# Kernel tuning notes

Measured on AMD Instinct MI355X. Metric: run time of the kernel, lower is better.

The kernel has to match this reference:

```python
import jax, jax.numpy as jnp
import numpy as np

CONF_THRES = 0.2   # from __init__ default
IOU_THRES = 0.6    # from __init__ default
MAX_WH = 4096.0    # class-offset for multi-class NMS (yolov7 convention)
TOPK = 2048        # pre-NMS candidates per image
MAX_DET = 300      # max detections per image (yolov7 default)
B, N, NC = 8, 25200, 80


def setup_inputs() -> dict:
    key = jax.random.key(0)
    k1, k2, k3 = jax.random.split(key, 3)
    # decoded predictions: [cx, cy, w, h, obj, cls_0..cls_79]
    xywh = jax.random.uniform(k1, (B, N, 4)) * jnp.array([640.0, 640.0, 120.0, 120.0])
    obj = jax.random.uniform(k2, (B, N, 1))
    cls = jax.random.uniform(k3, (B, N, NC))
    preds = jnp.concatenate([xywh, obj, cls], axis=-1)  # [B, N, 85]
    return {"preds": preds}


def _xywh2xyxy(xywh):
    cx, cy, w, h = xywh[..., 0], xywh[..., 1], xywh[..., 2], xywh[..., 3]
    return jnp.stack([cx - w * 0.5, cy - h * 0.5, cx + w * 0.5, cy + h * 0.5], axis=-1)


def _box_iou(a, b):
    # a: [K,4], b: [K,4] -> [K,K] pairwise IoU
    area_a = (a[:, 2] - a[:, 0]) * (a[:, 3] - a[:, 1])
    area_b = (b[:, 2] - b[:, 0]) * (b[:, 3] - b[:, 1])
    lt = jnp.maximum(a[:, None, :2], b[None, :, :2])  # [K,K,2]
    rb = jnp.minimum(a[:, None, 2:], b[None, :, 2:])
    wh = jnp.clip(rb - lt, 0.0)
    inter = wh[..., 0] * wh[..., 1]
    return inter / (area_a[:, None] + area_b[None, :] - inter + 1e-9)


def _nms_single(pred):
    # pred: [N, 5+NC]
    boxes = _xywh2xyxy(pred[:, :4])                 # [N,4]
    scores_all = pred[:, 5:] * pred[:, 4:5]         # obj * cls  [N,NC]
    conf = jnp.max(scores_all, axis=-1)             # best-class conf
    cls_id = jnp.argmax(scores_all, axis=-1)
    scores = jnp.where(conf > CONF_THRES, conf, 0.0)

    # pre-NMS top-k candidates (sorted descending)
    top_scores, idx = jax.lax.top_k(scores, TOPK)
    top_boxes = boxes[idx]                          # [K,4]
    top_cls = cls_id[idx]                           # [K]
    top_valid = top_scores > CONF_THRES

    # per-class NMS via class offset so cross-class boxes never overlap
    offset_boxes = top_boxes + (top_cls.astype(top_boxes.dtype) * MAX_WH)[:, None]
    iou = _box_iou(offset_boxes, offset_boxes)      # [K,K]

    # greedy NMS over score-sorted candidates
    def body(i, state):
        keep, suppressed = state
        k_i = top_valid[i] & jnp.logical_not(suppressed[i])
        keep = keep.at[i].set(k_i)
        sup_new = suppressed | (k_i & (iou[i] > IOU_THRES))
        sup_new = sup_new.at[i].set(suppressed[i])  # never self-suppress
        return keep, sup_new

    keep, _ = jax.lax.fori_loop(
        0, TOPK, body,
        (jnp.zeros(TOPK, dtype=bool), jnp.zeros(TOPK, dtype=bool)))

    # take top MAX_DET kept detections
    keep_scores = jnp.where(keep, top_scores, -1.0)
    det_scores, det_idx = jax.lax.top_k(keep_scores, MAX_DET)
    det = jnp.concatenate(
        [top_boxes[det_idx],
         det_scores[:, None],
         top_cls[det_idx].astype(pred.dtype)[:, None]], axis=-1)  # [MAX_DET,6]
    det = jnp.where((det_scores > 0.0)[:, None], det, 0.0)
    return det


def reference(preds):
    # preds: [B, N, 5+NC] -> [B, MAX_DET, 6] (x1,y1,x2,y2,conf,cls), zero-padded
    return jax.vmap(_nms_single)(preds)
```

## Files before the change

kernel.cpp:

```cpp
#include <hip/hip_runtime.h>

#define BATCH 8
#define NPRED 25200
#define NCLS 80
#define ROWW 85
#define TOPKK 2048
#define MAXDET 300
#define CANDMAX 4096
#define NBUCKET 4096
#define CONF_T 0.2f
#define IOU_T 0.6f
#define CLS_OFF 4096.0f

#define MASKN 384
#define MCH (MASKN / 64)
#define MW 13

typedef unsigned long long u64;
typedef unsigned int u32;

__device__ __forceinline__ int bucket_of_key(u64 k) {
    float sc = __uint_as_float((u32)(k >> 32));
    int bkt = (int)(sc * (float)NBUCKET);
    return (bkt > NBUCKET - 1) ? (NBUCKET - 1) : bkt;
}

__global__ __launch_bounds__(256) void k_score(
    const float* __restrict__ preds,
    u64* __restrict__ keys,
    unsigned char* __restrict__ cls8,
    u32* __restrict__ hist_g)
{
    __shared__ float4 rows4[64 * ROWW / 4 + 4];
    const int t = threadIdx.x;
    const int lane = t & 63;
    const int wave = t >> 6;
    const size_t rowbase = (size_t)blockIdx.x * 64;
    const float4* src = reinterpret_cast<const float4*>(preds + rowbase * ROWW);

    for (int q = wave; q < 21; q += 4) {
        __builtin_amdgcn_global_load_lds(
            (const __attribute__((address_space(1))) void*)(src + q * 64 + lane),
            (__attribute__((address_space(3))) void*)(rows4 + q * 64),
            16, 0, 0);
    }
    if (t < 16) rows4[1344 + t] = src[1344 + t];
    __syncthreads();

    const float* rows = reinterpret_cast<const float*>(rows4);
    const int r = t >> 2;
    const int j = t & 3;
    const float* p = rows + r * ROWW;
    const float obj = p[4];

    float best = -1.0f;
    int bi = 0;
    #pragma unroll
    for (int tt = 0; tt < 20; ++tt) {
        int c = j + 4 * tt;
        float s = __fmul_rn(obj, p[5 + c]);
        if (s > best) { best = s; bi = c; }
    }
    #pragma unroll
    for (int d = 1; d <= 2; d <<= 1) {
        float os = __shfl_xor(best, d);
        int oi = __shfl_xor(bi, d);
        if (os > best || (os == best && oi < bi)) { best = os; bi = oi; }
    }

    if (j == 0) {
        unsigned gid = (unsigned)rowbase + r;
        u64 key = 0ull;
        if (best > CONF_T) {
            key = ((u64)__float_as_uint(best) << 32) | (0xFFFFFFFFu - (gid % NPRED));
        }
        keys[gid] = key;
        cls8[gid] = (unsigned char)bi;
        if (key) {
            atomicAdd(&hist_g[(gid / NPRED) * NBUCKET + bucket_of_key(key)], 1u);
        }
    }
}

__global__ __launch_bounds__(1024) void k_scan(
    const u32* __restrict__ hist_g,
    u32* __restrict__ bstart_g,
    u32* __restrict__ balloc_g,
    int* __restrict__ tb_g,
    u32* __restrict__ stored_g)
{
    __shared__ u32 wtot[16];
    __shared__ u32 wsuf[16];
    __shared__ int s_tb;
    __shared__ u32 s_stored;

    const int b = blockIdx.x;
    const int t = threadIdx.x;
    const int lane = t & 63;
    const int wave = t >> 6;
    const u32* H = hist_g + (size_t)b * NBUCKET;

    u32 h0 = H[4 * t], h1 = H[4 * t + 1], h2 = H[4 * t + 2], h3 = H[4 * t + 3];
    u32 ps = h0 + h1 + h2 + h3;

    u32 v = ps;
    #pragma unroll
    for (int off = 1; off < 64; off <<= 1) {
        u32 u2 = __shfl_down(v, off);
        if (lane + off < 64) v += u2;
    }
    if (lane == 0) wtot[wave] = v;
    __syncthreads();
    if (t < 16) {
        u32 w = wtot[t];
        u32 s = w;
        #pragma unroll
        for (int off = 1; off < 16; off <<= 1) {
            u32 u2 = __shfl_down(s, off);
            if (t + off < 16) s += u2;
        }
        wsuf[t] = s - w;
    }
    if (t == 0) s_tb = 0;
    __syncthreads();
    u32 suffix_t = v + wsuf[wave];
    u32 snext = suffix_t - ps;

    u32 b3 = snext;
    u32 b2 = b3 + h3;
    u32 b1 = b2 + h2;
    u32 b0 = b1 + h1;
    const size_t B0 = (size_t)b * NBUCKET;
    bstart_g[B0 + 4 * t + 0] = b0;
    bstart_g[B0 + 4 * t + 1] = b1;
    bstart_g[B0 + 4 * t + 2] = b2;
    bstart_g[B0 + 4 * t + 3] = b3;
    balloc_g[B0 + 4 * t + 0] = b0;
    balloc_g[B0 + 4 * t + 1] = b1;
    balloc_g[B0 + 4 * t + 2] = b2;
    balloc_g[B0 + 4 * t + 3] = b3;

    if (t == 0) s_stored = (suffix_t < (u32)CANDMAX) ? suffix_t : (u32)CANDMAX;
    __syncthreads();
    {
        u32 c3 = b3 + h3, c2 = b2 + h2, c1 = b1 + h1, c0 = b0 + h0;
        if (c3 >= TOPKK && b3 < TOPKK) { s_tb = 4 * t + 3; s_stored = (c3 < (u32)CANDMAX) ? c3 : (u32)CANDMAX; }
        if (c2 >= TOPKK && b2 < TOPKK) { s_tb = 4 * t + 2; s_stored = (c2 < (u32)CANDMAX) ? c2 : (u32)CANDMAX; }
        if (c1 >= TOPKK && b1 < TOPKK) { s_tb = 4 * t + 1; s_stored = (c1 < (u32)CANDMAX) ? c1 : (u32)CANDMAX; }
        if (c0 >= TOPKK && b0 < TOPKK) { s_tb = 4 * t + 0; s_stored = (c0 < (u32)CANDMAX) ? c0 : (u32)CANDMAX; }
    }
    __syncthreads();
    if (t == 0) { tb_g[b] = s_tb; stored_g[b] = s_stored; }
}

__global__ __launch_bounds__(256) void k_compact(
    const u64* __restrict__ keys,
    u32* __restrict__ balloc_g,
    const int* __restrict__ tb_g,
    u64* __restrict__ cand_g)
{
    unsigned gid = blockIdx.x * 256 + threadIdx.x;
    if (gid >= BATCH * NPRED) return;
    u64 k = keys[gid];
    if (!k) return;
    int b = gid / NPRED;
    int bkt = bucket_of_key(k);
    if (bkt < tb_g[b]) return;
    u32 slot = atomicAdd(&balloc_g[(size_t)b * NBUCKET + bkt], 1u);
    if (slot < CANDMAX) cand_g[(size_t)b * CANDMAX + slot] = k;
}

struct RankPhase {
    u32 histL[NBUCKET];
    u32 bstartL[NBUCKET];
};
struct NmsPhase {
    u32 masks32[MASKN * MW];
    float4 cbx[MASKN];
    float carea[MASKN];
    float4 kb[MAXDET];
};

__global__ __launch_bounds__(1024) void k_finish(
    const float* __restrict__ preds,
    const unsigned char* __restrict__ cls8,
    const u32* __restrict__ hist_g,
    const u32* __restrict__ bstart_g,
    const int* __restrict__ tb_g,
    const u32* __restrict__ stored_g,
    const u64* __restrict__ cand_g,
    float* __restrict__ out)
{
    __shared__ union { RankPhase rk; NmsPhase nms; } u;
    __shared__ u64 candL[CANDMAX];
    __shared__ unsigned short rank2cand[TOPKK];
    __shared__ float4 sbox[MASKN];
    __shared__ float sscore[MASKN];
    __shared__ float scls[MASKN];
    __shared__ u64 validw[MCH];

    const int b = blockIdx.x;
    const int t = threadIdx.x;
    const int lane = t & 63;
    const int wave = t >> 6;
    float* ob = out + (size_t)b * MAXDET * 6;
    const u32 stored = stored_g[b];
    const int tb = tb_g[b];

    for (int i = tb + t; i < NBUCKET; i += 1024) {
        u.rk.histL[i] = hist_g[(size_t)b * NBUCKET + i];
        u.rk.bstartL[i] = bstart_g[(size_t)b * NBUCKET + i];
    }
    for (int i = t; i < TOPKK; i += 1024) rank2cand[i] = 0xFFFFu;
    for (int i = t; i < CANDMAX; i += 1024)
        if ((u32)i < stored) candL[i] = cand_g[(size_t)b * CANDMAX + i];
    if (t < MASKN) {
        sbox[t] = make_float4(0.f, 0.f, 0.f, 0.f);
        sscore[t] = 0.f;
        scls[t] = 0.f;
    }
    __syncthreads();

    for (u32 i = t; i < stored; i += 1024) {
        u64 k = candL[i];
        int bkt = bucket_of_key(k);
        u32 base = u.rk.bstartL[bkt];
        u32 end = base + u.rk.histL[bkt];
        if (end > stored) end = stored;
        u32 r = base;
        for (u32 jx = base; jx < end; ++jx) r += (candL[jx] > k) ? 1u : 0u;
        if (r < TOPKK) rank2cand[r] = (unsigned short)i;
        if (r < MASKN) {
            float sc = __uint_as_float((u32)(k >> 32));
            unsigned idx = 0xFFFFFFFFu - (u32)(k & 0xFFFFFFFFu);
            const float* p = preds + ((size_t)b * NPRED + idx) * ROWW;
            float cx = p[0], cy = p[1], w = p[2], h = p[3];
            float hw = __fmul_rn(w, 0.5f);
            float hh = __fmul_rn(h, 0.5f);
            sbox[r] = make_float4(__fsub_rn(cx, hw), __fsub_rn(cy, hh),
                                  __fadd_rn(cx, hw), __fadd_rn(cy, hh));
            sscore[r] = sc;
            scls[r] = (float)cls8[(size_t)b * NPRED + idx];
        }
    }
    __syncthreads();

    if (t < MASKN) {
        float sc = sscore[t];
        float cl = scls[t];
        float4 bb = sbox[t];
        float off = __fmul_rn(cl, CLS_OFF);
        float4 obx = make_float4(__fadd_rn(bb.x, off), __fadd_rn(bb.y, off),
                                 __fadd_rn(bb.z, off), __fadd_rn(bb.w, off));
        u.nms.cbx[t] = obx;
        u.nms.carea[t] = __fmul_rn(__fsub_rn(obx.z, obx.x), __fsub_rn(obx.w, obx.y));
        u64 vb = __ballot(sc > CONF_T);
        if (lane == 0) validw[wave] = vb;
    }
    __syncthreads();

    for (int tu = 0; tu < 3; ++tu) {
        int uidx = wave + 16 * tu;
        if (uidx >= 42) break;
        int q, s;
        if (uidx < 12)      { q = 0; s = uidx; }
        else if (uidx < 22) { q = 1; s = uidx - 12 + 2; }
        else if (uidx < 30) { q = 2; s = uidx - 22 + 4; }
        else if (uidx < 36) { q = 3; s = uidx - 30 + 6; }
        else if (uidx < 40) { q = 4; s = uidx - 36 + 8; }
        else                { q = 5; s = uidx - 40 + 10; }

        const int r = q * 64 + lane;
        const float4 me = u.nms.cbx[r];
        const float aA = u.nms.carea[r];
        const int j0 = s * 32;
        u32 acc = 0u;
        #pragma unroll 8
        for (int jj = 0; jj < 32; ++jj) {
            const int jx = j0 + jj;
            float4 cb = u.nms.cbx[jx];
            float lx = fmaxf(me.x, cb.x), ly = fmaxf(me.y, cb.y);
            float rx = fminf(me.z, cb.z), ry = fminf(me.w, cb.w);
            float iw = fmaxf(__fsub_rn(rx, lx), 0.0f);
            float ih = fmaxf(__fsub_rn(ry, ly), 0.0f);
            float inter = __fmul_rn(iw, ih);
            float denom = __fadd_rn(__fsub_rn(__fadd_rn(aA, u.nms.carea[jx]), inter), 1e-9f);
            bool sv = inter > __fmul_rn(IOU_T, denom);
            acc |= ((u32)sv) << jj;
        }
        if (s == 2 * q || s == 2 * q + 1) {
            int shift = r - j0;
            u32 dm = (shift < 0) ? ~0u : ((shift >= 31) ? 0u : (~0u << (shift + 1)));
            acc &= dm;
        }
        u.nms.masks32[r * MW + s] = acc;
    }
    __syncthreads();
    if (wave != 0) return;

    const u64 below = (lane == 0) ? 0ull : (~0ull >> (64 - lane));
    u64 S[MCH];
    #pragma unroll
    for (int w = 0; w < MCH; ++w) S[w] = 0ull;
    int nk = 0;
    bool done = false, allfull = true;

    #pragma unroll
    for (int c = 0; c < MCH; ++c) {
        if (done) break;
        u64 vw = validw[c];
        u64 eligible = vw & ~S[c];
        const int rbase = (c * 64 + lane) * MW;
        u64 Mu = ((u64)u.nms.masks32[rbase + 2 * c + 1] << 32) |
                 (u64)u.nms.masks32[rbase + 2 * c];
        bool elig = (eligible >> lane) & 1ull;
        if (eligible) {
            int cap = MAXDET - nk;
            u64 edge = __ballot(elig && ((Mu & eligible) != 0ull));
            u64 keptm;
            if (edge == 0ull) {
                int rank = __popcll(eligible & below);
                keptm = __ballot(elig && (rank < cap));
            } else {
                u64 km = 0ull, supm = 0ull;
                int cnt = 0;
                for (int m = 0; m < 64 && cnt < cap; ++m) {
                    if (!((eligible >> m) & 1ull)) continue;
                    if ((supm >> m) & 1ull) continue;
                    km |= 1ull << m;
                    ++cnt;
                    supm |= __shfl(Mu, m);
                }
                keptm = km;
            }
            if ((keptm >> lane) & 1ull) {
                int pos = nk + __popcll(keptm & below);
                int i = c * 64 + lane;
                float4 bb = sbox[i];
                u.nms.kb[pos] = u.nms.cbx[i];
                float* row = ob + pos * 6;
                row[0] = bb.x; row[1] = bb.y; row[2] = bb.z; row[3] = bb.w;
                row[4] = sscore[i]; row[5] = scls[i];
            }
            nk += __popcll(keptm);
            if (nk >= MAXDET) {
                done = true;
            } else if (keptm) {
                for (int w = c + 1; w < MCH; ++w) {
                    u64 v2 = ((keptm >> lane) & 1ull)
                        ? (((u64)u.nms.masks32[rbase + 2 * w + 1] << 32) |
                           (u64)u.nms.masks32[rbase + 2 * w])
                        : 0ull;
                    v2 |= __shfl_xor(v2, 1);  v2 |= __shfl_xor(v2, 2);
                    v2 |= __shfl_xor(v2, 4);  v2 |= __shfl_xor(v2, 8);
                    v2 |= __shfl_xor(v2, 16); v2 |= __shfl_xor(v2, 32);
                    S[w] |= v2;
                }
            }
        }
        if (vw != ~0ull) { allfull = false; break; }
    }

    if (!done && allfull && nk < MAXDET) {
        __threadfence_block();
        for (int c = MCH; c < TOPKK / 64; ++c) {
            int r = c * 64 + lane;
            unsigned short ci = rank2cand[r];
            bool valid = (ci != 0xFFFFu);
            u64 validmask = __ballot(valid);
            if (validmask == 0ull) break;

            float sc = 0.f, cl = 0.f;
            float bx1 = 0.f, by1 = 0.f, bx2 = 0.f, by2 = 0.f;
            if (valid) {
                u64 k = candL[ci];
                sc = __uint_as_float((u32)(k >> 32));
                unsigned idx = 0xFFFFFFFFu - (u32)(k & 0xFFFFFFFFu);
                const float* p = preds + ((size_t)b * NPRED + idx) * ROWW;
                float cx = p[0], cy = p[1], w = p[2], h = p[3];
                float hw = __fmul_rn(w, 0.5f);
                float hh = __fmul_rn(h, 0.5f);
                bx1 = __fsub_rn(cx, hw); by1 = __fsub_rn(cy, hh);
                bx2 = __fadd_rn(cx, hw); by2 = __fadd_rn(cy, hh);
                cl = (float)cls8[(size_t)b * NPRED + idx];
            }
            float off = __fmul_rn(cl, CLS_OFF);
            float x1 = __fadd_rn(bx1, off), y1 = __fadd_rn(by1, off);
            float x2 = __fadd_rn(bx2, off), y2 = __fadd_rn(by2, off);
            float areaA = __fmul_rn(__fsub_rn(x2, x1), __fsub_rn(y2, y1));

            bool sup = false;
            for (int jx = 0; jx < nk; ++jx) {
                float4 k4 = u.nms.kb[jx];
                float lx = fmaxf(x1, k4.x), ly = fmaxf(y1, k4.y);
                float rx = fminf(x2, k4.z), ry = fminf(y2, k4.w);
                float iw = fmaxf(__fsub_rn(rx, lx), 0.0f);
                float ih = fmaxf(__fsub_rn(ry, ly), 0.0f);
                float inter = __fmul_rn(iw, ih);
                float areaB = __fmul_rn(__fsub_rn(k4.z, k4.x), __fsub_rn(k4.w, k4.y));
                float denom = __fadd_rn(__fsub_rn(__fadd_rn(areaA, areaB), inter), 1e-9f);
                if (inter > __fmul_rn(IOU_T, denom)) sup = true;
            }
            u64 supprev = __ballot(sup);

            u32 sb_lo = 0u, sb_hi = 0u;
            for (int m = 0; m < 64; ++m) {
                float mx1 = __shfl(x1, m), my1 = __shfl(y1, m);
                float mx2 = __shfl(x2, m), my2 = __shfl(y2, m);
                float lx = fmaxf(x1, mx1), ly = fmaxf(y1, my1);
                float rx = fminf(x2, mx2), ry = fminf(y2, my2);
                float iw = fmaxf(__fsub_rn(rx, lx), 0.0f);
                float ih = fmaxf(__fsub_rn(ry, ly), 0.0f);
                float inter = __fmul_rn(iw, ih);
                float areaB = __fmul_rn(__fsub_rn(mx2, mx1), __fsub_rn(my2, my1));
                float denom = __fadd_rn(__fsub_rn(__fadd_rn(areaA, areaB), inter), 1e-9f);
                bool s = (m != lane) && (inter > __fmul_rn(IOU_T, denom));
                if (m < 32) sb_lo |= ((u32)s) << m;
                else        sb_hi |= ((u32)s) << (m - 32);
            }

            u64 eligible = validmask & ~supprev;
            u64 mysb = (((u64)sb_hi << 32) | (u64)sb_lo);
            bool iselig = (eligible >> lane) & 1ull;
            u64 edgeball = __ballot(iselig && ((mysb & eligible & below) != 0ull));

            u64 keptm;
            int cap = MAXDET - nk;
            if (edgeball == 0ull) {
                int rank = __popcll(eligible & below);
                keptm = __ballot(iselig && (rank < cap));
            } else {
                u64 km = 0ull;
                int cnt = 0;
                for (int m = 0; m < 64 && cnt < cap; ++m) {
                    if (!((validmask >> m) & 1ull)) break;
                    if ((supprev >> m) & 1ull) continue;
                    u32 mlo = (u32)__shfl((int)sb_lo, m);
                    u32 mhi = (u32)__shfl((int)sb_hi, m);
                    u64 supby = (((u64)mhi << 32) | (u64)mlo);
                    if (supby & km) continue;
                    km |= 1ull << m;
                    ++cnt;
                }
                keptm = km;
            }

            if ((keptm >> lane) & 1ull) {
                int pos = nk + __popcll(keptm & below);
                u.nms.kb[pos] = make_float4(x1, y1, x2, y2);
                float* row = ob + pos * 6;
                row[0] = bx1; row[1] = by1; row[2] = bx2; row[3] = by2;
                row[4] = sc;  row[5] = cl;
            }
            __threadfence_block();
            nk += __popcll(keptm);
            if (nk >= MAXDET) break;
            if (validmask != ~0ull) break;
        }
    }

    for (int x = nk * 6 + lane; x < MAXDET * 6; x += 64) ob[x] = 0.0f;
}

extern "C" void kernel_launch(void* const* d_in, const int* in_sizes, int n_in,
                              void* d_out, int out_size, void* d_ws, size_t ws_size,
                              hipStream_t stream) {
    const float* preds = (const float*)d_in[0];
    float* out = (float*)d_out;

    u32* hist_g   = (u32*)d_ws;
    u32* bstart_g = hist_g + BATCH * NBUCKET;
    u32* balloc_g = bstart_g + BATCH * NBUCKET;
    int* tb_g     = (int*)(balloc_g + BATCH * NBUCKET);
    u32* stored_g = (u32*)(tb_g + 8);
    u64* keys     = (u64*)(stored_g + 8);
    unsigned char* cls8 = (unsigned char*)(keys + BATCH * NPRED);
    u64* cand_g   = (u64*)(cls8 + BATCH * NPRED);

    hipMemsetAsync(hist_g, 0, (size_t)BATCH * NBUCKET * sizeof(u32), stream);

    hipLaunchKernelGGL(k_score, dim3(BATCH * NPRED / 64), dim3(256), 0, stream,
                       preds, keys, cls8, hist_g);
    hipLaunchKernelGGL(k_scan, dim3(BATCH), dim3(1024), 0, stream,
                       hist_g, bstart_g, balloc_g, tb_g, stored_g);
    hipLaunchKernelGGL(k_compact, dim3((BATCH * NPRED + 255) / 256), dim3(256), 0, stream,
                       keys, balloc_g, tb_g, cand_g);
    hipLaunchKernelGGL(k_finish, dim3(BATCH), dim3(1024), 0, stream,
                       preds, cls8, hist_g, bstart_g, tb_g, stored_g, cand_g, out);
}
```

Measured before the change: 64.87 us.

## Build per-image score histogram in LDS inside scan kernel, drop global atomics and memset

Moves the bucket histogram from global atomics in k_score into shared-memory atomics inside k_scan, which rereads the keys per image. This removes the hipMemsetAsync launch and the global atomic traffic. k_compact now handles two keys per thread with 16-byte loads. k_finish derives bucket end positions from neighbouring bstart entries instead of loading the histogram. The trade-off is that k_scan runs on only 8 blocks and must stream about 200 KB of keys each, which may serialize work that was previously spread across the whole grid.

```diff
diff --git a/kernel.cpp b/kernel.cpp
--- a/kernel.cpp
+++ b/kernel.cpp
@@ -28,8 +28,7 @@
 __global__ __launch_bounds__(256) void k_score(
     const float* __restrict__ preds,
     u64* __restrict__ keys,
-    unsigned char* __restrict__ cls8,
-    u32* __restrict__ hist_g)
+    unsigned char* __restrict__ cls8)
 {
     __shared__ float4 rows4[64 * ROWW / 4 + 4];
     const int t = threadIdx.x;
@@ -76,19 +75,17 @@
         }
         keys[gid] = key;
         cls8[gid] = (unsigned char)bi;
-        if (key) {
-            atomicAdd(&hist_g[(gid / NPRED) * NBUCKET + bucket_of_key(key)], 1u);
-        }
     }
 }
 
 __global__ __launch_bounds__(1024) void k_scan(
-    const u32* __restrict__ hist_g,
+    const u64* __restrict__ keys,
     u32* __restrict__ bstart_g,
     u32* __restrict__ balloc_g,
     int* __restrict__ tb_g,
     u32* __restrict__ stored_g)
 {
+    __shared__ u32 histL[NBUCKET];
     __shared__ u32 wtot[16];
     __shared__ u32 wsuf[16];
     __shared__ int s_tb;
@@ -98,9 +95,21 @@
     const int t = threadIdx.x;
     const int lane = t & 63;
     const int wave = t >> 6;
-    const u32* H = hist_g + (size_t)b * NBUCKET;
-
-    u32 h0 = H[4 * t], h1 = H[4 * t + 1], h2 = H[4 * t + 2], h3 = H[4 * t + 3];
+
+    for (int i = t; i < NBUCKET; i += 1024) histL[i] = 0u;
+    __syncthreads();
+
+    const uint4* k4 = reinterpret_cast<const uint4*>(keys + (size_t)b * NPRED);
+    for (int i = t; i < NPRED / 2; i += 1024) {
+        uint4 v = k4[i];
+        u64 ka = ((u64)v.y << 32) | v.x;
+        u64 kb = ((u64)v.w << 32) | v.z;
+        if (ka) atomicAdd(&histL[bucket_of_key(ka)], 1u);
+        if (kb) atomicAdd(&histL[bucket_of_key(kb)], 1u);
+    }
+    __syncthreads();
+
+    u32 h0 = histL[4 * t], h1 = histL[4 * t + 1], h2 = histL[4 * t + 2], h3 = histL[4 * t + 3];
     u32 ps = h0 + h1 + h2 + h3;
 
     u32 v = ps;
@@ -159,19 +168,30 @@
     const int* __restrict__ tb_g,
     u64* __restrict__ cand_g)
 {
-    unsigned gid = blockIdx.x * 256 + threadIdx.x;
-    if (gid >= BATCH * NPRED) return;
-    u64 k = keys[gid];
-    if (!k) return;
-    int b = gid / NPRED;
-    int bkt = bucket_of_key(k);
-    if (bkt < tb_g[b]) return;
-    u32 slot = atomicAdd(&balloc_g[(size_t)b * NBUCKET + bkt], 1u);
-    if (slot < CANDMAX) cand_g[(size_t)b * CANDMAX + slot] = k;
+    unsigned i2 = blockIdx.x * 256 + threadIdx.x;
+    if (i2 >= BATCH * NPRED / 2) return;
+    uint4 v = reinterpret_cast<const uint4*>(keys)[i2];
+    int b = (int)(i2 / (NPRED / 2));
+    int tb = tb_g[b];
+    u64 ka = ((u64)v.y << 32) | v.x;
+    u64 kb = ((u64)v.w << 32) | v.z;
+    if (ka) {
+        int bkt = bucket_of_key(ka);
+        if (bkt >= tb) {
+            u32 slot = atomicAdd(&balloc_g[(size_t)b * NBUCKET + bkt], 1u);
+            if (slot < CANDMAX) cand_g[(size_t)b * CANDMAX + slot] = ka;
+        }
+    }
+    if (kb) {
+        int bkt = bucket_of_key(kb);
+        if (bkt >= tb) {
+            u32 slot = atomicAdd(&balloc_g[(size_t)b * NBUCKET + bkt], 1u);
+            if (slot < CANDMAX) cand_g[(size_t)b * CANDMAX + slot] = kb;
+        }
+    }
 }
 
 struct RankPhase {
-    u32 histL[NBUCKET];
     u32 bstartL[NBUCKET];
 };
 struct NmsPhase {
@@ -184,7 +204,6 @@
 __global__ __launch_bounds__(1024) void k_finish(
     const float* __restrict__ preds,
     const unsigned char* __restrict__ cls8,
-    const u32* __restrict__ hist_g,
     const u32* __restrict__ bstart_g,
     const int* __restrict__ tb_g,
     const u32* __restrict__ stored_g,
@@ -206,11 +225,10 @@
     float* ob = out + (size_t)b * MAXDET * 6;
     const u32 stored = stored_g[b];
     const int tb = tb_g[b];
-
-    for (int i = tb + t; i < NBUCKET; i += 1024) {
-        u.rk.histL[i] = hist_g[(size_t)b * NBUCKET + i];
+    const int tb2 = (tb > 0) ? tb - 1 : 0;
+
+    for (int i = tb2 + t; i < NBUCKET; i += 1024)
         u.rk.bstartL[i] = bstart_g[(size_t)b * NBUCKET + i];
-    }
     for (int i = t; i < TOPKK; i += 1024) rank2cand[i] = 0xFFFFu;
     for (int i = t; i < CANDMAX; i += 1024)
         if ((u32)i < stored) candL[i] = cand_g[(size_t)b * CANDMAX + i];
@@ -225,7 +243,7 @@
         u64 k = candL[i];
         int bkt = bucket_of_key(k);
         u32 base = u.rk.bstartL[bkt];
-        u32 end = base + u.rk.histL[bkt];
+        u32 end = (bkt == 0) ? stored : u.rk.bstartL[bkt - 1];
         if (end > stored) end = stored;
         u32 r = base;
         for (u32 jx = base; jx < end; ++jx) r += (candL[jx] > k) ? 1u : 0u;
@@ -468,23 +486,20 @@
     const float* preds = (const float*)d_in[0];
     float* out = (float*)d_out;
 
-    u32* hist_g   = (u32*)d_ws;
-    u32* bstart_g = hist_g + BATCH * NBUCKET;
+    u64* keys     = (u64*)d_ws;
+    u64* cand_g   = keys + (size_t)BATCH * NPRED;
+    u32* bstart_g = (u32*)(cand_g + (size_t)BATCH * CANDMAX);
     u32* balloc_g = bstart_g + BATCH * NBUCKET;
     int* tb_g     = (int*)(balloc_g + BATCH * NBUCKET);
     u32* stored_g = (u32*)(tb_g + 8);
-    u64* keys     = (u64*)(stored_g + 8);
-    unsigned char* cls8 = (unsigned char*)(keys + BATCH * NPRED);
-    u64* cand_g   = (u64*)(cls8 + BATCH * NPRED);
-
-    hipMemsetAsync(hist_g, 0, (size_t)BATCH * NBUCKET * sizeof(u32), stream);
+    unsigned char* cls8 = (unsigned char*)(stored_g + 8);
 
     hipLaunchKernelGGL(k_score, dim3(BATCH * NPRED / 64), dim3(256), 0, stream,
-                       preds, keys, cls8, hist_g);
+                       preds, keys, cls8);
     hipLaunchKernelGGL(k_scan, dim3(BATCH), dim3(1024), 0, stream,
-                       hist_g, bstart_g, balloc_g, tb_g, stored_g);
-    hipLaunchKernelGGL(k_compact, dim3((BATCH * NPRED + 255) / 256), dim3(256), 0, stream,
+                       keys, bstart_g, balloc_g, tb_g, stored_g);
+    hipLaunchKernelGGL(k_compact, dim3((BATCH * NPRED / 2 + 255) / 256), dim3(256), 0, stream,
                        keys, balloc_g, tb_g, cand_g);
     hipLaunchKernelGGL(k_finish, dim3(BATCH), dim3(1024), 0, stream,
-                       preds, cls8, hist_g, bstart_g, tb_g, stored_g, cand_g, out);
+                       preds, cls8, bstart_g, tb_g, stored_g, cand_g, out);
 }
```

New measurement: 56.01 us, median of 2. 13.7% less time.
